# Kernel optimization log

Hardware: AMD Instinct MI355X
Metric: run time of the kernel (lower is better)

## Reference

```python
import jax, jax.numpy as jnp
import numpy as np

N_NODES = 64
NUM_STEPS = 15
N_DP = 5
SLOPE = 25.0  # fast_sigmoid surrogate slope


def _spike(x):
    # forward Heaviside; surrogate grad only matters in bwd module
    return (x > 0).astype(x.dtype)


def _lif(x, mem, beta, thr):
    # snnTorch Leaky, reset_mechanism='subtract': reset from previous mem (detached)
    reset = jax.lax.stop_gradient((mem > thr).astype(x.dtype))
    mem = beta * mem + x - reset * thr
    spk = _spike(mem - thr)
    return spk, mem


def setup_inputs() -> dict:
    key = jax.random.key(0)
    ks = jax.random.split(key, 16)
    B = 2048
    def xavier(k, shape):
        fan_in, fan_out = shape
        lim = float(np.sqrt(6.0 / (fan_in + fan_out)))
        return jax.random.uniform(k, shape, jnp.float32, -lim, lim)
    return {
        "L_norm": jax.random.normal(ks[0], (B, N_NODES, N_NODES), jnp.float32),
        "X_seq": jax.random.normal(ks[1], (B, NUM_STEPS, N_NODES, 1), jnp.float32),
        "W_proj": xavier(ks[2], (1, 16)),   "b_proj": jnp.zeros((16,), jnp.float32),
        "W_gcn1": xavier(ks[3], (16, 32)),  "b_gcn1": jnp.zeros((32,), jnp.float32),
        "W_skip1": xavier(ks[4], (16, 32)), "b_skip1": jnp.zeros((32,), jnp.float32),
        "W_gcn2": xavier(ks[5], (32, 64)),  "b_gcn2": jnp.zeros((64,), jnp.float32),
        "W_skip2": xavier(ks[6], (32, 64)), "b_skip2": jnp.zeros((64,), jnp.float32),
        "W_c1": xavier(ks[7], (N_NODES * 64, 128)), "b_c1": jnp.zeros((128,), jnp.float32),
        "W_c2": xavier(ks[8], (128, 4)),    "b_c2": jnp.zeros((4,), jnp.float32),
    }


def reference(L_norm, X_seq, W_proj, b_proj, W_gcn1, b_gcn1, W_skip1, b_skip1,
              W_gcn2, b_gcn2, W_skip2, b_skip2, W_c1, b_c1, W_c2, b_c2):
    B = X_seq.shape[0]

    def hr_gcn(x, mems, Wg, bg, Ws, bs, betas, thrs):
        # dense Laplacian conv: (L @ (x W)) + b, plus triple LIF + linear skip
        cur = jnp.einsum("bnm,bmf->bnf", L_norm, x @ Wg) + bg
        spk_a, m_a = _lif(cur, mems[0], betas[0], thrs[0])
        spk_n, m_n = _lif(cur, mems[1], betas[1], thrs[1])
        spk_m, m_m = _lif(cur, mems[2], betas[2], thrs[2])
        spk_out = spk_a + spk_n + spk_m + (x @ Ws + bs)
        return spk_out, (m_a, m_n, m_m)

    z = lambda f: jnp.zeros((B, N_NODES, f), jnp.float32)
    carry0 = ((z(32),) * 3, (z(64),) * 3, z(64))

    def step(carry, x_t):
        mems1, mems2, mem_li = carry
        x = x_t @ W_proj + b_proj                      # [B, N, 16]
        spk1, mems1 = hr_gcn(x, mems1, W_gcn1, b_gcn1, W_skip1, b_skip1,
                             (0.8, 0.9, 0.95), (0.8, 1.0, 1.5))
        spk2, mems2 = hr_gcn(spk1, mems2, W_gcn2, b_gcn2, W_skip2, b_skip2,
                             (0.8, 0.9, 0.95), (0.8, 1.0, 1.5))
        mem_li = 0.9 * mem_li + spk2                   # Leaky, reset 'none'
        pot = mem_li.reshape(B, -1)                    # [B, N*64]
        return (mems1, mems2, mem_li), pot

    xs = jnp.swapaxes(X_seq, 0, 1)                     # [T, B, N, 1]
    _, pots = jax.lax.scan(step, carry0, xs)
    potentials = jnp.swapaxes(pots, 0, 1)              # [B, T, N*64]

    # DP decoder (dropout = identity in eval)
    dp_feat = potentials[:, -N_DP:, :].mean(axis=1) - potentials[:, :N_DP, :].mean(axis=1)
    h = jax.nn.relu(dp_feat @ W_c1 + b_c1)
    return h @ W_c2 + b_c2
```

## Files before the change

### kernel.cpp

```cpp
#include <hip/hip_runtime.h>
#include <hip/hip_bf16.h>


typedef __attribute__((ext_vector_type(8))) short s16x8;
typedef __attribute__((ext_vector_type(4))) float f32x4;
#define MFMA16(a, b, c) __builtin_amdgcn_mfma_f32_16x16x32_bf16(a, b, c, 0, 0, 0)

__device__ __forceinline__ short f2bs(float x) {
  union { __hip_bfloat16 h; short s; } u; u.h = __float2bfloat16(x); return u.s;
}
__device__ __forceinline__ float bs2f(short s) {
  union { short s; __hip_bfloat16 h; } u; u.s = s; return __bfloat162float(u.h);
}

#define LIF_STEP(mem, beta, thr, cur, spksum)                \
  {                                                          \
    float r_ = ((mem) > (thr)) ? (thr) : 0.0f;               \
    (mem) = (beta) * (mem) + (cur) - r_;                     \
    (spksum) += (((mem) - (thr)) > 0.0f) ? 1.0f : 0.0f;      \
  }

#define LFS 68
#define RS  36

__global__ __launch_bounds__(512, 2)
void hrsnn_main(const float* __restrict__ Lg,  const float* __restrict__ Xg,
                const float* __restrict__ Wp,  const float* __restrict__ bp,
                const float* __restrict__ Wg1, const float* __restrict__ bg1,
                const float* __restrict__ Ws1, const float* __restrict__ bs1,
                const float* __restrict__ Wg2, const float* __restrict__ bg2,
                const float* __restrict__ Ws2, const float* __restrict__ bs2,
                unsigned int* __restrict__ dp_out)
{
  __shared__ __align__(16) float UBUF[4608];
  float* const Lf    = UBUF;
  float* const S1row = UBUF;
  float* const Mrow  = UBUF + 2304;
  __shared__ __align__(16) short WgF[4 * 3 * 64 * 8];
  __shared__ __align__(16) unsigned int XtHL[960];
  __shared__ __align__(16) float Xtf[960];
  __shared__ float LxS[64], LsumS[64];
  __shared__ float u1A[32], cb1A[32], us1v[32], cs1v[32];
  __shared__ float u2gA[64], c2gA[64], u2sA[64], cs2A[64];

  const int tid = threadIdx.x;
  const int b = blockIdx.x;
  const int l = tid & 63, w = tid >> 6;
  const int p = w >> 1, h = w & 1;
  const int q = l >> 4, c = l & 15;
  const int R = 16 * p;

  const float* Lb = Lg + (size_t)b * 4096;
#pragma unroll
  for (int k = 0; k < 2; k++) {
    const int i4 = tid + 512 * k;
    const float4 v = *(const float4*)&Lb[i4 * 4];
    *(float4*)&Lf[(i4 >> 4) * LFS + (i4 & 15) * 4] = v;
  }
  const float* Xb = Xg + (size_t)b * 960;
  for (int i = tid; i < 960; i += 512) {
    const float x = Xb[i];
    const short hs = f2bs(x);
    const short ls = f2bs(x - bs2f(hs));
    XtHL[i] = ((unsigned int)(unsigned short)hs << 16) | (unsigned short)ls;
    Xtf[i] = x;
  }
  if (tid < 32) {
    const int f = tid;
    float a = 0.f, bb = 0.f, cc = 0.f, d = 0.f;
    for (int k = 0; k < 16; k++) {
      const float wp = Wp[k], bpv = bp[k];
      const float wg = Wg1[k * 32 + f], ws = Ws1[k * 32 + f];
      a += wp * wg; bb += bpv * wg;
      cc += wp * ws; d += bpv * ws;
    }
    u1A[f] = a; cb1A[f] = bb;
    us1v[f] = cc; cs1v[f] = d + bs1[f];
  }
  __syncthreads();

  {
    const int n = tid >> 3, o = tid & 7;
    const float4 a4 = *(const float4*)&Lf[n * LFS + 8 * o];
    const float4 b4 = *(const float4*)&Lf[n * LFS + 8 * o + 4];
    float ps = a4.x + a4.y + a4.z + a4.w + b4.x + b4.y + b4.z + b4.w;
    ps += __shfl_xor(ps, 1, 64);
    ps += __shfl_xor(ps, 2, 64);
    ps += __shfl_xor(ps, 4, 64);
    if (o == 0) LsumS[n] = ps;
  }
  s16x8 Lh[2], Lm[2], Ll[2];
#pragma unroll
  for (int s = 0; s < 2; s++) {
    const float* rp = &Lf[(R + c) * LFS + 32 * s + 8 * q];
    const float4 v0 = *(const float4*)rp;
    const float4 v1 = *(const float4*)(rp + 4);
    float v[8] = {v0.x, v0.y, v0.z, v0.w, v1.x, v1.y, v1.z, v1.w};
#pragma unroll
    for (int j = 0; j < 8; j++) {
      const short hh = f2bs(v[j]);       const float r1 = v[j] - bs2f(hh);
      const short mm = f2bs(r1);         const float r2 = r1 - bs2f(mm);
      Lh[s][j] = hh; Lm[s][j] = mm; Ll[s][j] = f2bs(r2);
    }
  }
  {
    const int tt = w & 3;
    float v[8];
#pragma unroll
    for (int j = 0; j < 8; j++) v[j] = Wg2[(8 * q + j) * 64 + 16 * tt + c];
    if (w < 4) {
      s16x8 fh, fm;
#pragma unroll
      for (int j = 0; j < 8; j++) {
        const short hh = f2bs(v[j]);
        fh[j] = hh; fm[j] = f2bs(v[j] - bs2f(hh));
      }
      *(s16x8*)&WgF[((tt * 3 + 0) * 64 + l) * 8] = fh;
      *(s16x8*)&WgF[((tt * 3 + 1) * 64 + l) * 8] = fm;
    } else {
      s16x8 fl;
#pragma unroll
      for (int j = 0; j < 8; j++) {
        const short hh = f2bs(v[j]);     const float r1 = v[j] - bs2f(hh);
        const short mm = f2bs(r1);       const float r2 = r1 - bs2f(mm);
        fl[j] = f2bs(r2);
      }
      *(s16x8*)&WgF[((tt * 3 + 2) * 64 + l) * 8] = fl;
    }
  }
  s16x8 WsH[2], WsL[2];
#pragma unroll
  for (int i = 0; i < 2; i++) {
    const int g0 = 32 * h + 16 * i;
#pragma unroll
    for (int j = 0; j < 8; j++) {
      const float x = Ws2[(8 * q + j) * 64 + g0 + c];
      const short hh = f2bs(x);
      WsH[i][j] = hh; WsL[i][j] = f2bs(x - bs2f(hh));
    }
  }
  __syncthreads();

  if (tid < 64) {
    const int g = tid;
    float a = 0.f, bb = 0.f, cc = 0.f, d = 0.f;
    for (int f = 0; f < 32; f++) {
      const float wg = Wg2[f * 64 + g], ws = Ws2[f * 64 + g];
      a += us1v[f] * wg; bb += cs1v[f] * wg;
      cc += us1v[f] * ws; d += cs1v[f] * ws;
    }
    u2gA[g] = a; c2gA[g] = bb; u2sA[g] = cc; cs2A[g] = d + bs2[g];
  }
  __syncthreads();

  float u2g2[2], u2s2[2], cs22[2], c2c[2][4];
#pragma unroll
  for (int i = 0; i < 2; i++) {
    const int g = 32 * h + 16 * i + c;
    u2g2[i] = u2gA[g]; u2s2[i] = u2sA[g]; cs22[i] = cs2A[g];
    const float cg = c2gA[g], bg = bg2[g];
#pragma unroll
    for (int r = 0; r < 4; r++) c2c[i][r] = LsumS[R + 4 * q + r] * cg + bg;
  }
  const int f1 = tid & 31, nb = tid >> 5;
  const float u1f = u1A[f1];
  float k1c[4];
  {
    const float cb = cb1A[f1], bg = bg1[f1];
#pragma unroll
    for (int j = 0; j < 4; j++) k1c[j] = LsumS[nb + 16 * j] * cb + bg;
  }

  float m1a[4], m1n[4], m1m[4];
#pragma unroll
  for (int j = 0; j < 4; j++) { m1a[j] = 0.f; m1n[j] = 0.f; m1m[j] = 0.f; }
  float m2a[2][4], m2n[2][4], m2m[2][4], mli[2][4], dpa[2][4];
#pragma unroll
  for (int i = 0; i < 2; i++)
#pragma unroll
    for (int r = 0; r < 4; r++) {
      m2a[i][r] = 0.f; m2n[i][r] = 0.f; m2m[i][r] = 0.f;
      mli[i][r] = 0.f; dpa[i][r] = 0.f;
    }

  const f32x4 fz = {0.f, 0.f, 0.f, 0.f};
  __syncthreads();

  for (int t = 0; t < 15; t++) {
    f32x4 lx = fz;
#pragma unroll
    for (int s = 0; s < 2; s++) {
      const unsigned int* xw = &XtHL[t * 64 + 32 * s + 8 * q];
      const uint4 w0 = *(const uint4*)xw;
      const uint4 w1 = *(const uint4*)(xw + 4);
      unsigned int wv[8] = {w0.x, w0.y, w0.z, w0.w, w1.x, w1.y, w1.z, w1.w};
      s16x8 bh, bl;
#pragma unroll
      for (int j = 0; j < 8; j++) {
        bh[j] = (short)(wv[j] >> 16);
        bl[j] = (short)(wv[j] & 0xffff);
      }
      lx = MFMA16(Lh[s], bh, lx);
      lx = MFMA16(Lm[s], bh, lx);
      lx = MFMA16(Lh[s], bl, lx);
    }
    if (h == 0 && c == 0) {
#pragma unroll
      for (int r = 0; r < 4; r++) LxS[R + 4 * q + r] = lx[r];
    }
    __syncthreads();

#pragma unroll
    for (int j = 0; j < 4; j++) {
      const int n = nb + 16 * j;
      const float cur = LxS[n] * u1f + k1c[j];
      float ss = 0.f;
      LIF_STEP(m1a[j], 0.8f, 0.8f, cur, ss);
      LIF_STEP(m1n[j], 0.9f, 1.0f, cur, ss);
      LIF_STEP(m1m[j], 0.95f, 1.5f, cur, ss);
      S1row[n * RS + f1] = ss;
    }
    __syncthreads();

    f32x4 macc = fz;
#pragma unroll
    for (int s = 0; s < 2; s++) {
      s16x8 bS;
#pragma unroll
      for (int j = 0; j < 8; j++)
        bS[j] = f2bs(S1row[(32 * s + 8 * q + j) * RS + 16 * h + c]);
      macc = MFMA16(Lh[s], bS, macc);
      macc = MFMA16(Lm[s], bS, macc);
      macc = MFMA16(Ll[s], bS, macc);
    }
#pragma unroll
    for (int r = 0; r < 4; r++) Mrow[(R + 4 * q + r) * RS + 16 * h + c] = macc[r];

    f32x4 sacc[2];
    {
      const float* rp = &S1row[(R + c) * RS + 8 * q];
      const float4 v0 = *(const float4*)rp;
      const float4 v1 = *(const float4*)(rp + 4);
      const float v[8] = {v0.x, v0.y, v0.z, v0.w, v1.x, v1.y, v1.z, v1.w};
      s16x8 aS;
#pragma unroll
      for (int j = 0; j < 8; j++) aS[j] = f2bs(v[j]);
#pragma unroll
      for (int i = 0; i < 2; i++) {
        sacc[i] = MFMA16(aS, WsH[i], fz);
        sacc[i] = MFMA16(aS, WsL[i], sacc[i]);
      }
    }
    __syncthreads();

    s16x8 aMh, aMm, aMl;
    {
      const float* rp = &Mrow[(R + c) * RS + 8 * q];
      const float4 v0 = *(const float4*)rp;
      const float4 v1 = *(const float4*)(rp + 4);
      const float v[8] = {v0.x, v0.y, v0.z, v0.w, v1.x, v1.y, v1.z, v1.w};
#pragma unroll
      for (int j = 0; j < 8; j++) {
        const short hh = f2bs(v[j]);     const float r1 = v[j] - bs2f(hh);
        const short mm = f2bs(r1);       const float r2 = r1 - bs2f(mm);
        aMh[j] = hh; aMm[j] = mm; aMl[j] = f2bs(r2);
      }
    }
    float xtn[4];
#pragma unroll
    for (int r = 0; r < 4; r++) xtn[r] = Xtf[t * 64 + R + 4 * q + r];

#pragma unroll
    for (int i = 0; i < 2; i++) {
      const int tt = 2 * h + i;
      const s16x8 bGh = *(const s16x8*)&WgF[((tt * 3 + 0) * 64 + l) * 8];
      const s16x8 bGm = *(const s16x8*)&WgF[((tt * 3 + 1) * 64 + l) * 8];
      const s16x8 bGl = *(const s16x8*)&WgF[((tt * 3 + 2) * 64 + l) * 8];
      f32x4 cacc = fz;
      cacc = MFMA16(aMh, bGh, cacc);
      cacc = MFMA16(aMh, bGm, cacc);
      cacc = MFMA16(aMm, bGh, cacc);
      cacc = MFMA16(aMh, bGl, cacc);
      cacc = MFMA16(aMm, bGm, cacc);
      cacc = MFMA16(aMl, bGh, cacc);
#pragma unroll
      for (int r = 0; r < 4; r++) {
        const float cur2 = cacc[r] + lx[r] * u2g2[i] + c2c[i][r];
        float ss = 0.f;
        LIF_STEP(m2a[i][r], 0.8f, 0.8f, cur2, ss);
        LIF_STEP(m2n[i][r], 0.9f, 1.0f, cur2, ss);
        LIF_STEP(m2m[i][r], 0.95f, 1.5f, cur2, ss);
        const float spk2 = ss + sacc[i][r] + xtn[r] * u2s2[i] + cs22[i];
        mli[i][r] = 0.9f * mli[i][r] + spk2;
      }
    }
    if (t < 5) {
#pragma unroll
      for (int i = 0; i < 2; i++)
#pragma unroll
        for (int r = 0; r < 4; r++) dpa[i][r] -= mli[i][r];
    } else if (t >= 10) {
#pragma unroll
      for (int i = 0; i < 2; i++)
#pragma unroll
        for (int r = 0; r < 4; r++) dpa[i][r] += mli[i][r];
    }
  }

  unsigned int* dpb = dp_out + (size_t)b * 4096;
#pragma unroll
  for (int i = 0; i < 2; i++) {
    const int g = 32 * h + 16 * i + c;
#pragma unroll
    for (int r = 0; r < 4; r++) {
      const int n = R + 4 * q + r;
      const float v = dpa[i][r] * 0.2f;
      const short hh = f2bs(v);
      const short ll = f2bs(v - bs2f(hh));
      dpb[n * 64 + g] = ((unsigned int)(unsigned short)hh << 16) | (unsigned short)ll;
    }
  }
}


#define DEC_STEP(S, CA0, CA1)                                          \
  {                                                                    \
    const unsigned int av[8] = {(CA0).x, (CA0).y, (CA0).z, (CA0).w,    \
                                (CA1).x, (CA1).y, (CA1).z, (CA1).w};   \
    s16x8 Ah, Al, Bh, Bl;                                              \
    _Pragma("unroll")                                                  \
    for (int j = 0; j < 8; j++) {                                      \
      Ah[j] = (short)(av[j] >> 16);                                    \
      Al[j] = (short)(av[j] & 0xffff);                                 \
      const float x = bcol2[(32 * (S) + j) * 128];                     \
      const short hh = f2bs(x);                                        \
      Bh[j] = hh; Bl[j] = f2bs(x - bs2f(hh));                          \
    }                                                                  \
    acc = MFMA16(Ah, Bh, acc);                                         \
    acc = MFMA16(Al, Bh, acc);                                         \
    acc = MFMA16(Ah, Bl, acc);                                         \
  }

#define DEC_SLOT(S, BUF, NXT)                                          \
  {                                                                    \
    const uint4 c0 = BUF[0], c1 = BUF[1];                              \
    if ((NXT) < 64) {                                                  \
      BUF[0] = *(const uint4*)(arow2 + 32 * (NXT));                    \
      BUF[1] = *(const uint4*)(arow2 + 32 * (NXT) + 4);                \
    }                                                                  \
    DEC_STEP(S, c0, c1);                                               \
  }

__global__ __launch_bounds__(512, 2)
void hrsnn_decoder(const unsigned int* __restrict__ dpq, const float* __restrict__ W1,
                   const float* __restrict__ b1, const float* __restrict__ W2,
                   const float* __restrict__ b2, float* __restrict__ out)
{
  __shared__ __align__(16) float Hp[2][16][68];
  const int tid = threadIdx.x;
  const int l = tid & 63, w = tid >> 6;
  const int tw = w & 3, kh = w >> 2;
  const int g  = blockIdx.x >> 1;
  const int hb = blockIdx.x & 1;
  const int q = l >> 4, c = l & 15;
  const int col = 64 * hb + 16 * tw + c;

  const unsigned int* arow2 = dpq + (size_t)(g * 16 + c) * 4096 + 2048 * kh + 8 * q;
  const float* bcol2 = W1 + (size_t)(2048 * kh + 8 * q) * 128 + col;

  f32x4 acc = {0.f, 0.f, 0.f, 0.f};
  uint4 A0[2], A1[2], A2[2], A3[2];
  A0[0] = *(const uint4*)(arow2);       A0[1] = *(const uint4*)(arow2 + 4);
  A1[0] = *(const uint4*)(arow2 + 32);  A1[1] = *(const uint4*)(arow2 + 36);
  A2[0] = *(const uint4*)(arow2 + 64);  A2[1] = *(const uint4*)(arow2 + 68);
  A3[0] = *(const uint4*)(arow2 + 96);  A3[1] = *(const uint4*)(arow2 + 100);
  for (int sl = 0; sl < 64; sl += 4) {
    DEC_SLOT(sl,     A0, sl + 4);
    DEC_SLOT(sl + 1, A1, sl + 5);
    DEC_SLOT(sl + 2, A2, sl + 6);
    DEC_SLOT(sl + 3, A3, sl + 7);
  }

#pragma unroll
  for (int r = 0; r < 4; r++) Hp[kh][4 * q + r][16 * tw + c] = acc[r];
  __syncthreads();

  if (tid < 64) {
    const int i = tid >> 2, o = tid & 3;
    float s = 0.5f * b2[o];
    const float* b1h = b1 + 64 * hb;
    const float* w2 = W2 + (64 * hb) * 4 + o;
    for (int k = 0; k < 64; k++) {
      float hv = Hp[0][i][k] + Hp[1][i][k] + b1h[k];
      hv = hv > 0.f ? hv : 0.f;
      s += hv * w2[k * 4];
    }
    atomicAdd(&out[(size_t)(g * 16 + i) * 4 + o], s);
  }
}

extern "C" void kernel_launch(void* const* d_in, const int* in_sizes, int n_in,
                              void* d_out, int out_size, void* d_ws, size_t ws_size,
                              hipStream_t stream)
{
  const float* Lg  = (const float*)d_in[0];
  const float* Xg  = (const float*)d_in[1];
  const float* Wp  = (const float*)d_in[2];
  const float* bp  = (const float*)d_in[3];
  const float* Wg1 = (const float*)d_in[4];
  const float* bg1 = (const float*)d_in[5];
  const float* Ws1 = (const float*)d_in[6];
  const float* bs1 = (const float*)d_in[7];
  const float* Wg2 = (const float*)d_in[8];
  const float* bg2 = (const float*)d_in[9];
  const float* Ws2 = (const float*)d_in[10];
  const float* bs2 = (const float*)d_in[11];
  const float* W1  = (const float*)d_in[12];
  const float* b1  = (const float*)d_in[13];
  const float* W2  = (const float*)d_in[14];
  const float* b2  = (const float*)d_in[15];

  unsigned int* dpq = (unsigned int*)d_ws;
  float* out = (float*)d_out;

  hipLaunchKernelGGL(hrsnn_main, dim3(2048), dim3(512), 0, stream,
                     Lg, Xg, Wp, bp, Wg1, bg1, Ws1, bs1, Wg2, bg2, Ws2, bs2, dpq);
  hipMemsetAsync(out, 0, (size_t)2048 * 4 * sizeof(float), stream);
  hipLaunchKernelGGL(hrsnn_decoder, dim3(256), dim3(512), 0, stream,
                     dpq, W1, b1, W2, b2, out);
}
```

Before: 439.2 us.

## Prepack W1 into split-bf16 transposed layout and rewrite decoder without atomics

Result: slower. 462.0 us (+5.2%).

```diff
diff --git a/kernel.cpp b/kernel.cpp
--- a/kernel.cpp
+++ b/kernel.cpp
@@ -322,6 +322,120 @@
   }
 }
 
+__global__ __launch_bounds__(512, 2)
+void w1_pack(const float* __restrict__ W1, unsigned int* __restrict__ W1F)
+{
+  __shared__ unsigned int T[32][129];
+  const int tid = threadIdx.x;
+  const int k0 = blockIdx.x * 32;
+#pragma unroll
+  for (int p = 0; p < 8; p++) {
+    const int lin = p * 512 + tid;
+    const int kk = lin >> 7, colr = lin & 127;
+    const float x = W1[(size_t)(k0 + kk) * 128 + colr];
+    const short hh = f2bs(x);
+    const short ll = f2bs(x - bs2f(hh));
+    T[kk][colr] = ((unsigned int)(unsigned short)hh << 16) | (unsigned short)ll;
+  }
+  __syncthreads();
+  const int colw = tid >> 2, j = tid & 3;
+#pragma unroll
+  for (int u = 0; u < 8; u++) {
+    const int kk = 8 * j + u;
+    W1F[(size_t)colw * 4096 + k0 + kk] = T[kk][colw];
+  }
+}
+
+#define AST 36
+
+__global__ __launch_bounds__(512, 2)
+void hrsnn_decoder_v4(const unsigned int* __restrict__ dpq,
+                      const unsigned int* __restrict__ W1F,
+                      const float* __restrict__ b1, const float* __restrict__ W2,
+                      const float* __restrict__ b2, float* __restrict__ out)
+{
+  __shared__ __align__(16) unsigned int Abuf[2][8 * 16 * AST];
+  __shared__ __align__(16) float Hs[16][132];
+  const int tid = threadIdx.x;
+  const int l = tid & 63, tw = tid >> 6;
+  const int g = blockIdx.x;
+  const int q = l >> 4, c = l & 15;
+  const int col = 16 * tw + c;
+
+  const int srow = l >> 2, su0 = (l & 3) * 8;
+  const unsigned int* astage = dpq + (size_t)(g * 16 + srow) * 4096 + su0;
+  const int sdst = (tw * 16 + srow) * AST + su0;
+  const unsigned int* brow = W1F + (size_t)col * 4096 + 8 * q;
+
+  uint4 Br[4][2];
+#pragma unroll
+  for (int i = 0; i < 4; i++) {
+    Br[i][0] = *(const uint4*)(brow + 32 * i);
+    Br[i][1] = *(const uint4*)(brow + 32 * i + 4);
+  }
+  uint4 a0 = *(const uint4*)(astage + 32 * tw);
+  uint4 a1 = *(const uint4*)(astage + 32 * tw + 4);
+  {
+    unsigned int* dst = &Abuf[0][sdst];
+    *(uint4*)dst = a0; *(uint4*)(dst + 4) = a1;
+  }
+  __syncthreads();
+
+  f32x4 acc = {0.f, 0.f, 0.f, 0.f};
+  for (int ch = 0; ch < 16; ch++) {
+    if (ch < 15) {
+      const int gs = (ch + 1) * 8 + tw;
+      a0 = *(const uint4*)(astage + 32 * gs);
+      a1 = *(const uint4*)(astage + 32 * gs + 4);
+    }
+    const unsigned int* abase = &Abuf[ch & 1][0];
+#pragma unroll
+    for (int s = 0; s < 8; s++) {
+      const unsigned int* ap = abase + (s * 16 + c) * AST + 8 * q;
+      const uint4 av0 = *(const uint4*)ap;
+      const uint4 av1 = *(const uint4*)(ap + 4);
+      const uint4 bv0 = Br[s & 3][0], bv1 = Br[s & 3][1];
+      const int gs2 = ch * 8 + s + 4;
+      if (gs2 < 128) {
+        Br[s & 3][0] = *(const uint4*)(brow + 32 * gs2);
+        Br[s & 3][1] = *(const uint4*)(brow + 32 * gs2 + 4);
+      }
+      const unsigned int av[8] = {av0.x, av0.y, av0.z, av0.w, av1.x, av1.y, av1.z, av1.w};
+      const unsigned int bv[8] = {bv0.x, bv0.y, bv0.z, bv0.w, bv1.x, bv1.y, bv1.z, bv1.w};
+      s16x8 Ah, Al, Bh, Bl;
+#pragma unroll
+      for (int j = 0; j < 8; j++) {
+        Ah[j] = (short)(av[j] >> 16);
+        Al[j] = (short)(av[j] & 0xffff);
+        Bh[j] = (short)(bv[j] >> 16);
+        Bl[j] = (short)(bv[j] & 0xffff);
+      }
+      acc = MFMA16(Ah, Bh, acc);
+      acc = MFMA16(Al, Bh, acc);
+      acc = MFMA16(Ah, Bl, acc);
+    }
+    if (ch < 15) {
+      unsigned int* dst = &Abuf[(ch + 1) & 1][sdst];
+      *(uint4*)dst = a0; *(uint4*)(dst + 4) = a1;
+    }
+    __syncthreads();
+  }
+
+  const float bk = b1[col];
+#pragma unroll
+  for (int r = 0; r < 4; r++) {
+    const float hv = acc[r] + bk;
+    Hs[4 * q + r][col] = hv > 0.f ? hv : 0.f;
+  }
+  __syncthreads();
+
+  if (tid < 64) {
+    const int i = tid >> 2, o = tid & 3;
+    float s = b2[o];
+    for (int k = 0; k < 128; k++) s += Hs[i][k] * W2[k * 4 + o];
+    out[(size_t)(g * 16 + i) * 4 + o] = s;
+  }
+}
 
 #define DEC_STEP(S, CA0, CA1)                                          \
   {                                                                    \
@@ -422,10 +536,20 @@
 
   unsigned int* dpq = (unsigned int*)d_ws;
   float* out = (float*)d_out;
+  const size_t DPQ_U = (size_t)2048 * 4096;
+  const size_t W1F_U = (size_t)128 * 4096;
+  const bool prepack = ws_size >= (DPQ_U + W1F_U) * sizeof(unsigned int);
 
   hipLaunchKernelGGL(hrsnn_main, dim3(2048), dim3(512), 0, stream,
                      Lg, Xg, Wp, bp, Wg1, bg1, Ws1, bs1, Wg2, bg2, Ws2, bs2, dpq);
-  hipMemsetAsync(out, 0, (size_t)2048 * 4 * sizeof(float), stream);
-  hipLaunchKernelGGL(hrsnn_decoder, dim3(256), dim3(512), 0, stream,
-                     dpq, W1, b1, W2, b2, out);
-}
+  if (prepack) {
+    unsigned int* W1F = dpq + DPQ_U;
+    hipLaunchKernelGGL(w1_pack, dim3(128), dim3(512), 0, stream, W1, W1F);
+    hipLaunchKernelGGL(hrsnn_decoder_v4, dim3(128), dim3(512), 0, stream,
+                       dpq, W1F, b1, W2, b2, out);
+  } else {
+    hipMemsetAsync(out, 0, (size_t)2048 * 4 * sizeof(float), stream);
+    hipLaunchKernelGGL(hrsnn_decoder, dim3(256), dim3(512), 0, stream,
+                       dpq, W1, b1, W2, b2, out);
+  }
+}
```

## Process two batch elements per 1024-thread block sharing weight fragments

Applied to the files above, without the earlier changes.

New measurement: 788.0 us. 1.79x slower.

```diff
diff --git a/kernel.cpp b/kernel.cpp
--- a/kernel.cpp
+++ b/kernel.cpp
@@ -23,7 +23,7 @@
 #define LFS 68
 #define RS  36
 
-__global__ __launch_bounds__(512, 2)
+__global__ __launch_bounds__(1024, 4)
 void hrsnn_main(const float* __restrict__ Lg,  const float* __restrict__ Xg,
                 const float* __restrict__ Wp,  const float* __restrict__ bp,
                 const float* __restrict__ Wg1, const float* __restrict__ bg1,
@@ -32,41 +32,44 @@
                 const float* __restrict__ Ws2, const float* __restrict__ bs2,
                 unsigned int* __restrict__ dp_out)
 {
-  __shared__ __align__(16) float UBUF[4608];
-  float* const Lf    = UBUF;
-  float* const S1row = UBUF;
-  float* const Mrow  = UBUF + 2304;
+  __shared__ __align__(16) float UBUF[2][4608];
   __shared__ __align__(16) short WgF[4 * 3 * 64 * 8];
-  __shared__ __align__(16) unsigned int XtHL[960];
-  __shared__ __align__(16) float Xtf[960];
-  __shared__ float LxS[64], LsumS[64];
-  __shared__ float u1A[32], cb1A[32], us1v[32], cs1v[32];
-  __shared__ float u2gA[64], c2gA[64], u2sA[64], cs2A[64];
+  __shared__ __align__(16) unsigned int XtHL[2][960];
+  __shared__ __align__(16) float Xtf[2][960];
+  __shared__ float LxS[2][64], LsumS[2][64];
+  __shared__ float u1A[2][32], cb1A[2][32], us1v[2][32], cs1v[2][32];
+  __shared__ float u2gA[2][64], c2gA[2][64], u2sA[2][64], cs2A[2][64];
 
   const int tid = threadIdx.x;
-  const int b = blockIdx.x;
-  const int l = tid & 63, w = tid >> 6;
+  const int hw = tid >> 9;
+  const int t5 = tid & 511;
+  const int b = blockIdx.x * 2 + hw;
+  const int l = t5 & 63, w = t5 >> 6;
   const int p = w >> 1, h = w & 1;
   const int q = l >> 4, c = l & 15;
   const int R = 16 * p;
 
+  float* const Lf    = UBUF[hw];
+  float* const S1row = UBUF[hw];
+  float* const Mrow  = UBUF[hw] + 2304;
+
   const float* Lb = Lg + (size_t)b * 4096;
 #pragma unroll
   for (int k = 0; k < 2; k++) {
-    const int i4 = tid + 512 * k;
+    const int i4 = t5 + 512 * k;
     const float4 v = *(const float4*)&Lb[i4 * 4];
     *(float4*)&Lf[(i4 >> 4) * LFS + (i4 & 15) * 4] = v;
   }
   const float* Xb = Xg + (size_t)b * 960;
-  for (int i = tid; i < 960; i += 512) {
+  for (int i = t5; i < 960; i += 512) {
     const float x = Xb[i];
     const short hs = f2bs(x);
     const short ls = f2bs(x - bs2f(hs));
-    XtHL[i] = ((unsigned int)(unsigned short)hs << 16) | (unsigned short)ls;
-    Xtf[i] = x;
-  }
-  if (tid < 32) {
-    const int f = tid;
+    XtHL[hw][i] = ((unsigned int)(unsigned short)hs << 16) | (unsigned short)ls;
+    Xtf[hw][i] = x;
+  }
+  if (t5 < 32) {
+    const int f = t5;
     float a = 0.f, bb = 0.f, cc = 0.f, d = 0.f;
     for (int k = 0; k < 16; k++) {
       const float wp = Wp[k], bpv = bp[k];
@@ -74,20 +77,20 @@
       a += wp * wg; bb += bpv * wg;
       cc += wp * ws; d += bpv * ws;
     }
-    u1A[f] = a; cb1A[f] = bb;
-    us1v[f] = cc; cs1v[f] = d + bs1[f];
+    u1A[hw][f] = a; cb1A[hw][f] = bb;
+    us1v[hw][f] = cc; cs1v[hw][f] = d + bs1[f];
   }
   __syncthreads();
 
   {
-    const int n = tid >> 3, o = tid & 7;
+    const int n = t5 >> 3, o = t5 & 7;
     const float4 a4 = *(const float4*)&Lf[n * LFS + 8 * o];
     const float4 b4 = *(const float4*)&Lf[n * LFS + 8 * o + 4];
     float ps = a4.x + a4.y + a4.z + a4.w + b4.x + b4.y + b4.z + b4.w;
     ps += __shfl_xor(ps, 1, 64);
     ps += __shfl_xor(ps, 2, 64);
     ps += __shfl_xor(ps, 4, 64);
-    if (o == 0) LsumS[n] = ps;
+    if (o == 0) LsumS[hw][n] = ps;
   }
   s16x8 Lh[2], Lm[2], Ll[2];
 #pragma unroll
@@ -103,7 +106,7 @@
       Lh[s][j] = hh; Lm[s][j] = mm; Ll[s][j] = f2bs(r2);
     }
   }
-  {
+  if (hw == 0) {
     const int tt = w & 3;
     float v[8];
 #pragma unroll
@@ -141,15 +144,15 @@
   }
   __syncthreads();
 
-  if (tid < 64) {
-    const int g = tid;
+  if (t5 < 64) {
+    const int g = t5;
     float a = 0.f, bb = 0.f, cc = 0.f, d = 0.f;
     for (int f = 0; f < 32; f++) {
       const float wg = Wg2[f * 64 + g], ws = Ws2[f * 64 + g];
-      a += us1v[f] * wg; bb += cs1v[f] * wg;
-      cc += us1v[f] * ws; d += cs1v[f] * ws;
-    }
-    u2gA[g] = a; c2gA[g] = bb; u2sA[g] = cc; cs2A[g] = d + bs2[g];
+      a += us1v[hw][f] * wg; bb += cs1v[hw][f] * wg;
+      cc += us1v[hw][f] * ws; d += cs1v[hw][f] * ws;
+    }
+    u2gA[hw][g] = a; c2gA[hw][g] = bb; u2sA[hw][g] = cc; cs2A[hw][g] = d + bs2[g];
   }
   __syncthreads();
 
@@ -157,18 +160,18 @@
 #pragma unroll
   for (int i = 0; i < 2; i++) {
     const int g = 32 * h + 16 * i + c;
-    u2g2[i] = u2gA[g]; u2s2[i] = u2sA[g]; cs22[i] = cs2A[g];
-    const float cg = c2gA[g], bg = bg2[g];
-#pragma unroll
-    for (int r = 0; r < 4; r++) c2c[i][r] = LsumS[R + 4 * q + r] * cg + bg;
-  }
-  const int f1 = tid & 31, nb = tid >> 5;
-  const float u1f = u1A[f1];
+    u2g2[i] = u2gA[hw][g]; u2s2[i] = u2sA[hw][g]; cs22[i] = cs2A[hw][g];
+    const float cg = c2gA[hw][g], bg = bg2[g];
+#pragma unroll
+    for (int r = 0; r < 4; r++) c2c[i][r] = LsumS[hw][R + 4 * q + r] * cg + bg;
+  }
+  const int f1 = t5 & 31, nb = t5 >> 5;
+  const float u1f = u1A[hw][f1];
   float k1c[4];
   {
-    const float cb = cb1A[f1], bg = bg1[f1];
-#pragma unroll
-    for (int j = 0; j < 4; j++) k1c[j] = LsumS[nb + 16 * j] * cb + bg;
+    const float cb = cb1A[hw][f1], bg = bg1[f1];
+#pragma unroll
+    for (int j = 0; j < 4; j++) k1c[j] = LsumS[hw][nb + 16 * j] * cb + bg;
   }
 
   float m1a[4], m1n[4], m1m[4];
@@ -190,7 +193,7 @@
     f32x4 lx = fz;
 #pragma unroll
     for (int s = 0; s < 2; s++) {
-      const unsigned int* xw = &XtHL[t * 64 + 32 * s + 8 * q];
+      const unsigned int* xw = &XtHL[hw][t * 64 + 32 * s + 8 * q];
       const uint4 w0 = *(const uint4*)xw;
       const uint4 w1 = *(const uint4*)(xw + 4);
       unsigned int wv[8] = {w0.x, w0.y, w0.z, w0.w, w1.x, w1.y, w1.z, w1.w};
@@ -206,14 +209,14 @@
     }
     if (h == 0 && c == 0) {
 #pragma unroll
-      for (int r = 0; r < 4; r++) LxS[R + 4 * q + r] = lx[r];
+      for (int r = 0; r < 4; r++) LxS[hw][R + 4 * q + r] = lx[r];
     }
     __syncthreads();
 
 #pragma unroll
     for (int j = 0; j < 4; j++) {
       const int n = nb + 16 * j;
-      const float cur = LxS[n] * u1f + k1c[j];
+      const float cur = LxS[hw][n] * u1f + k1c[j];
       float ss = 0.f;
       LIF_STEP(m1a[j], 0.8f, 0.8f, cur, ss);
       LIF_STEP(m1n[j], 0.9f, 1.0f, cur, ss);
@@ -268,7 +271,7 @@
     }
     float xtn[4];
 #pragma unroll
-    for (int r = 0; r < 4; r++) xtn[r] = Xtf[t * 64 + R + 4 * q + r];
+    for (int r = 0; r < 4; r++) xtn[r] = Xtf[hw][t * 64 + R + 4 * q + r];
 
 #pragma unroll
     for (int i = 0; i < 2; i++) {
@@ -423,7 +426,7 @@
   unsigned int* dpq = (unsigned int*)d_ws;
   float* out = (float*)d_out;
 
-  hipLaunchKernelGGL(hrsnn_main, dim3(2048), dim3(512), 0, stream,
+  hipLaunchKernelGGL(hrsnn_main, dim3(1024), dim3(1024), 0, stream,
                      Lg, Xg, Wp, bp, Wg1, bg1, Ws1, bs1, Wg2, bg2, Ws2, bs2, dpq);
   hipMemsetAsync(out, 0, (size_t)2048 * 4 * sizeof(float), stream);
   hipLaunchKernelGGL(hrsnn_decoder, dim3(256), dim3(512), 0, stream,
```
